# Kernel optimization log

Measured on AMD Instinct MI355X. Metric: run time of the kernel, lower is better.

The kernel has to match this reference:

```python
import jax, jax.numpy as jnp
import numpy as np

# ---- static config (mirrors init_kwargs) ----
B, N, C_IN, C_OUT = 4, 8192, 128, 256
RATIO = 0.25
M = int(N * RATIO)          # sampled centers per cloud (fps ratio)
RADIUS = 0.1
MAX_NN = 64                 # max_num_neighbors
K = 16                      # num kernel points
D_MID = C_IN // 2           # pre_mlp: in_features -> in_features // 2
KP_EXTENT = RADIUS          # kernel-point influence extent (linear influence)


def setup_inputs() -> dict:
    key = jax.random.key(0)
    ks = jax.random.split(key, 10)
    x = jax.random.normal(ks[0], (B, N, C_IN), jnp.float32)
    pos = jax.random.uniform(ks[1], (B, N, 3), jnp.float32)  # unit cube
    W_pre = jax.random.normal(ks[2], (C_IN, D_MID), jnp.float32) / np.sqrt(C_IN).astype(np.float32)
    b_pre = jnp.zeros((D_MID,), jnp.float32)
    kp_pos = jax.random.normal(ks[3], (K, 3), jnp.float32) * (0.3 * RADIUS)
    kp_W = jax.random.normal(ks[4], (K, D_MID, D_MID), jnp.float32) / np.sqrt(D_MID * K).astype(np.float32)
    W_post = jax.random.normal(ks[5], (D_MID, C_OUT), jnp.float32) / np.sqrt(D_MID).astype(np.float32)
    b_post = jnp.zeros((C_OUT,), jnp.float32)
    W_sc = jax.random.normal(ks[6], (C_IN, C_OUT), jnp.float32) / np.sqrt(C_IN).astype(np.float32)
    b_sc = jnp.zeros((C_OUT,), jnp.float32)
    return dict(x=x, pos=pos, W_pre=W_pre, b_pre=b_pre, kp_pos=kp_pos, kp_W=kp_W,
                W_post=W_post, b_post=b_post, W_sc=W_sc, b_sc=b_sc)


def _fps(p):
    """Farthest point sampling on one cloud p:[N,3] -> idx:[M] (start at point 0)."""
    mind = jnp.sum((p - p[0]) ** 2, axis=-1)  # [N]
    def step(mind, _):
        i = jnp.argmax(mind).astype(jnp.int32)
        mind = jnp.minimum(mind, jnp.sum((p - p[i]) ** 2, axis=-1))
        return mind, i
    _, rest = jax.lax.scan(step, mind, None, length=M - 1)
    return jnp.concatenate([jnp.zeros((1,), jnp.int32), rest])


def reference(x, pos, W_pre, b_pre, kp_pos, kp_W, W_post, b_post, W_sc, b_sc):
    def _cloud(xb, pb):
        # xb:[N,C_IN], pb:[N,3]
        idx = _fps(pb)                                   # [M]
        centers = pb[idx]                                # [M,3]
        # radius neighbor search: nearest MAX_NN, mask to ball of RADIUS
        d2 = jnp.sum((centers[:, None, :] - pb[None, :, :]) ** 2, axis=-1)   # [M,N]
        neg_d2, nn_idx = jax.lax.top_k(-d2, MAX_NN)      # [M,MAX_NN]
        valid = (-neg_d2) <= RADIUS ** 2                 # [M,MAX_NN]
        # pre mlp then gather neighbor features (x_j)
        x_pre = xb @ W_pre + b_pre                       # [N,D_MID]
        x_j = x_pre[nn_idx]                              # [M,MAX_NN,D_MID]
        # kernel-point conv: linear influence of each kernel point
        rel = pb[nn_idx] - centers[:, None, :]           # [M,MAX_NN,3]
        dist = jnp.sqrt(jnp.sum((rel[:, :, None, :] - kp_pos[None, None, :, :]) ** 2, axis=-1) + 1e-12)  # [M,MAX_NN,K]
        infl = jnp.maximum(1.0 - dist / KP_EXTENT, 0.0) * valid[:, :, None]
        # aggregate (sum over neighbors) per kernel point, then contract with kernel weights
        s = jnp.einsum('mek,med->mkd', infl, x_j)        # [M,K,D_MID]
        feat = jnp.einsum('mkd,kdo->mo', s, kp_W)        # [M,D_MID]
        feat = feat @ W_post + b_post                    # [M,C_OUT]
        short = xb[idx] @ W_sc + b_sc                    # residual shortcut on sampled points
        return feat + short, centers

    out_feat, out_pos = jax.vmap(_cloud)(x, pos)         # [B,M,C_OUT], [B,M,3]
    return out_feat, out_pos
```

## Files before the change

kernel.cpp:

```cpp
#include <hip/hip_runtime.h>

#define B_    4
#define N_    8192
#define CIN   128
#define COUT  256
#define M_    2048
#define K_    16
#define DM    64
#define MAXNN 64
#define CAP   128
#define R2    0.01f
#define EXT   0.1f

__device__ __forceinline__ float d2_exact(float ax, float ay, float az,
                                          float bx, float by, float bz) {
    float dx = ax - bx, dy = ay - by, dz = az - bz;
    return __fadd_rn(__fadd_rn(__fmul_rn(dx, dx), __fmul_rn(dy, dy)), __fmul_rn(dz, dz));
}

#define DPP_STEP2(CTRL)                                                                   \
    {                                                                                     \
        unsigned tlo = (unsigned)__builtin_amdgcn_update_dpp(0, (int)klo, CTRL, 0xF, 0xF, true); \
        unsigned thi = (unsigned)__builtin_amdgcn_update_dpp(0, (int)khi, CTRL, 0xF, 0xF, true); \
        unsigned long long tk = ((unsigned long long)thi << 32) | tlo;                    \
        unsigned long long ck = ((unsigned long long)khi << 32) | klo;                    \
        if (tk > ck) { klo = tlo; khi = thi; }                                            \
    }

__global__ __launch_bounds__(512) void fps_kernel(const float* __restrict__ pos,
                                                  int* __restrict__ idx_out,
                                                  float* __restrict__ out_pos) {
    const int b = blockIdx.x;
    const int t = threadIdx.x;
    const float* pb = pos + (size_t)b * N_ * 3;

    __shared__ unsigned long long keyS[2][8];

    float px[16], py[16], pz[16], mind[16];
#pragma unroll
    for (int j = 0; j < 16; j++) {
        int n = t + j * 512;
        px[j] = pb[n * 3 + 0];
        py[j] = pb[n * 3 + 1];
        pz[j] = pb[n * 3 + 2];
        mind[j] = 1e30f;
    }
    float cx = pb[0], cy = pb[1], cz = pb[2];
    if (t == 0) {
        idx_out[b * M_ + 0] = 0;
        float* op = out_pos + ((size_t)(b * M_ + 0)) * 3;
        op[0] = cx; op[1] = cy; op[2] = cz;
    }

    for (int m = 1; m < M_; m++) {
        float bv = -1.0f; int bn = 0;
#pragma unroll
        for (int j = 0; j < 16; j++) {
#pragma clang fp contract(off)
            float dx = px[j] - cx, dy = py[j] - cy, dz = pz[j] - cz;
            float d = (dx * dx + dy * dy) + dz * dz;
            d = fminf(mind[j], d);
            mind[j] = d;
            if (d > bv) { bv = d; bn = t + j * 512; }
        }
        unsigned klo = 0xFFFFFFFFu - (unsigned)bn;
        unsigned khi = __float_as_uint(bv);

        DPP_STEP2(0x111)
        DPP_STEP2(0x112)
        DPP_STEP2(0x114)
        DPP_STEP2(0x118)
        DPP_STEP2(0x142)
        DPP_STEP2(0x143)

        const int buf = m & 1;
        if ((t & 63) == 63) {
            keyS[buf][t >> 6] = ((unsigned long long)khi << 32) | klo;
        }
        __syncthreads();
        unsigned long long k0 = keyS[buf][0];
#pragma unroll
        for (int w = 1; w < 8; w++) {
            unsigned long long kw = keyS[buf][w];
            if (kw > k0) k0 = kw;
        }
        const unsigned widx = 0xFFFFFFFFu - (unsigned)(k0 & 0xFFFFFFFFull);
        const float* cp = pb + (size_t)widx * 3;
        cx = cp[0]; cy = cp[1]; cz = cp[2];
        if (t == 0) {
            idx_out[b * M_ + m] = (int)widx;
            float* op = out_pos + ((size_t)(b * M_ + m)) * 3;
            op[0] = cx; op[1] = cy; op[2] = cz;
        }
    }
}

__global__ __launch_bounds__(256) void pre_kernel(const float* __restrict__ x,
                                                  const float* __restrict__ W,
                                                  const float* __restrict__ bvec,
                                                  float* __restrict__ xpre) {
    __shared__ float Ws[CIN * DM];
    __shared__ float xs[16][CIN];
    const int t = threadIdx.x;
    for (int i = t; i < CIN * DM; i += 256) Ws[i] = W[i];
    const size_t rowBase = (size_t)blockIdx.x * 16;
    for (int i = t; i < 16 * CIN; i += 256) {
        int r = i >> 7, c = i & 127;
        xs[r][c] = x[(rowBase + r) * CIN + c];
    }
    __syncthreads();
    const int col = t & 63, r0 = t >> 6;
    float acc[4];
    float bias = bvec[col];
#pragma unroll
    for (int rr = 0; rr < 4; rr++) acc[rr] = bias;
    for (int c = 0; c < CIN; c++) {
        float w = Ws[c * DM + col];
#pragma unroll
        for (int rr = 0; rr < 4; rr++) acc[rr] = fmaf(xs[r0 + 4 * rr][c], w, acc[rr]);
    }
#pragma unroll
    for (int rr = 0; rr < 4; rr++) xpre[(rowBase + r0 + 4 * rr) * DM + col] = acc[rr];
}

__global__ __launch_bounds__(256) void conv_kernel(const float* __restrict__ pos,
                                                   const float* __restrict__ x,
                                                   const float* __restrict__ xpre,
                                                   const int* __restrict__ idxs,
                                                   const float* __restrict__ kp_pos,
                                                   const float* __restrict__ kp_W,
                                                   const float* __restrict__ W_post,
                                                   const float* __restrict__ b_post,
                                                   const float* __restrict__ W_sc,
                                                   const float* __restrict__ b_sc,
                                                   float* __restrict__ out_feat) {
    const int blk = blockIdx.x;
    const int b = blk / M_;
    const int m = blk % M_;
    const int t = threadIdx.x;

    __shared__ int   nIdx[CAP];
    __shared__ float nD2[CAP];
    __shared__ int   cntS;
    __shared__ float infl[MAXNN][K_];
    __shared__ float xj[MAXNN][DM];
    __shared__ float sS[K_ * DM];
    __shared__ float featP[4][DM];
    __shared__ float xg[CIN];

    const float* pb = pos + (size_t)b * N_ * 3;
    const int ctr = idxs[b * M_ + m];
    const float cx = pb[ctr * 3 + 0], cy = pb[ctr * 3 + 1], cz = pb[ctr * 3 + 2];

    if (t == 0) cntS = 0;
    __syncthreads();

    for (int j = 0; j < N_ / 256; j++) {
        int n = j * 256 + t;
        float x0 = pb[n * 3 + 0], y0 = pb[n * 3 + 1], z0 = pb[n * 3 + 2];
        float d = d2_exact(x0, y0, z0, cx, cy, cz);
        if (d <= R2) {
            int p = atomicAdd(&cntS, 1);
            if (p < CAP) { nIdx[p] = n; nD2[p] = d; }
        }
    }
    __syncthreads();
    int cnt = cntS; if (cnt > CAP) cnt = CAP;
    if (cnt > MAXNN) {
        if (t == 0) {
            for (int s = 0; s < MAXNN; s++) {
                int best = s;
                for (int q = s + 1; q < cnt; q++) {
                    if (nD2[q] < nD2[best] || (nD2[q] == nD2[best] && nIdx[q] < nIdx[best])) best = q;
                }
                float td = nD2[best]; nD2[best] = nD2[s]; nD2[s] = td;
                int ti = nIdx[best]; nIdx[best] = nIdx[s]; nIdx[s] = ti;
            }
        }
        __syncthreads();
        cnt = MAXNN;
    }

    if (t < cnt) {
        int n = nIdx[t];
        float rx = pb[n * 3 + 0] - cx, ry = pb[n * 3 + 1] - cy, rz = pb[n * 3 + 2] - cz;
#pragma unroll
        for (int k = 0; k < K_; k++) {
            float dx = rx - kp_pos[k * 3 + 0];
            float dy = ry - kp_pos[k * 3 + 1];
            float dz = rz - kp_pos[k * 3 + 2];
            float dist = sqrtf(dx * dx + dy * dy + dz * dz + 1e-12f);
            infl[t][k] = fmaxf(1.0f - dist / EXT, 0.0f);
        }
    }
    for (int i = t; i < cnt * DM; i += 256) {
        int e = i >> 6, d = i & 63;
        xj[e][d] = xpre[((size_t)b * N_ + nIdx[e]) * DM + d];
    }
    __syncthreads();

#pragma unroll
    for (int p = 0; p < 4; p++) {
        int pair = t + p * 256;
        int k = pair >> 6, d = pair & 63;
        float acc = 0.f;
        for (int e = 0; e < cnt; e++) acc = fmaf(infl[e][k], xj[e][d], acc);
        sS[pair] = acc;
    }
    __syncthreads();

    {
        int dprime = t & 63, ks = t >> 6;
        float acc = 0.f;
        for (int k = ks * 4; k < ks * 4 + 4; k++) {
            const float* kw = kp_W + ((size_t)k * DM) * DM + dprime;
#pragma unroll
            for (int d = 0; d < DM; d++) acc = fmaf(sS[k * DM + d], kw[d * DM], acc);
        }
        featP[ks][dprime] = acc;
    }
    __syncthreads();
    if (t < DM) featP[0][t] = featP[0][t] + featP[1][t] + featP[2][t] + featP[3][t];
    if (t < CIN) xg[t] = x[((size_t)b * N_ + ctr) * CIN + t];
    __syncthreads();

    {
        const int o = t;
        float acc = b_post[o] + b_sc[o];
#pragma unroll 8
        for (int d = 0; d < DM; d++) acc = fmaf(featP[0][d], W_post[d * COUT + o], acc);
#pragma unroll 8
        for (int c = 0; c < CIN; c++) acc = fmaf(xg[c], W_sc[c * COUT + o], acc);
        out_feat[((size_t)(b * M_ + m)) * COUT + o] = acc;
    }
}

extern "C" void kernel_launch(void* const* d_in, const int* in_sizes, int n_in,
                              void* d_out, int out_size, void* d_ws, size_t ws_size,
                              hipStream_t stream) {
    const float* x      = (const float*)d_in[0];
    const float* pos    = (const float*)d_in[1];
    const float* W_pre  = (const float*)d_in[2];
    const float* b_pre  = (const float*)d_in[3];
    const float* kp_pos = (const float*)d_in[4];
    const float* kp_W   = (const float*)d_in[5];
    const float* W_post = (const float*)d_in[6];
    const float* b_post = (const float*)d_in[7];
    const float* W_sc   = (const float*)d_in[8];
    const float* b_sc   = (const float*)d_in[9];

    float* out_feat = (float*)d_out;
    float* out_pos  = (float*)d_out + (size_t)B_ * M_ * COUT;

    int*   idxs = (int*)d_ws;
    float* xpre = (float*)((char*)d_ws + 64 * 1024);

    fps_kernel<<<B_, 512, 0, stream>>>(pos, idxs, out_pos);
    pre_kernel<<<(B_ * N_) / 16, 256, 0, stream>>>(x, W_pre, b_pre, xpre);
    conv_kernel<<<B_ * M_, 256, 0, stream>>>(pos, x, xpre, idxs, kp_pos, kp_W,
                                             W_post, b_post, W_sc, b_sc, out_feat);
}
```

Before: 2.389 ms.

## Fuse pre-MLP into FPS launch, packed-float FPS, atomicMax reduction

Folds the pre-MLP GEMM into the FPS kernel launch as extra blocks, so the pre-MLP runs on idle CUs alongside the four serial FPS blocks and one launch is saved. Inside FPS, the distance update uses 2-wide float vectors, which can map to packed FP32 math. The per-iteration cross-wave reduction now uses a shared atomicMax on a rotating 4-slot buffer instead of eight stores followed by a serial max scan. The risks are LDS atomic contention and the need to reset slots correctly across iterations.

```diff
diff --git a/kernel.cpp b/kernel.cpp
--- a/kernel.cpp
+++ b/kernel.cpp
@@ -12,6 +12,8 @@
 #define R2    0.01f
 #define EXT   0.1f
 
+typedef float v2f __attribute__((ext_vector_type(2)));
+
 __device__ __forceinline__ float d2_exact(float ax, float ay, float az,
                                           float bx, float by, float bz) {
     float dx = ax - bx, dy = ay - by, dz = az - bz;
@@ -27,43 +29,83 @@
         if (tk > ck) { klo = tlo; khi = thi; }                                            \
     }
 
-__global__ __launch_bounds__(512) void fps_kernel(const float* __restrict__ pos,
-                                                  int* __restrict__ idx_out,
-                                                  float* __restrict__ out_pos) {
+__global__ __launch_bounds__(512, 2) void fps_pre_kernel(const float* __restrict__ pos,
+                                                         int* __restrict__ idx_out,
+                                                         float* __restrict__ out_pos,
+                                                         const float* __restrict__ x,
+                                                         const float* __restrict__ Wp,
+                                                         const float* __restrict__ bvec,
+                                                         float* __restrict__ xpre) {
+    __shared__ union {
+        unsigned long long keySlot[4];
+        struct { float Ws[CIN * DM]; float xs[32][CIN]; } p;
+    } sh;
+
+    const int t = threadIdx.x;
+
+    if (blockIdx.x >= 4) {
+        const size_t rowBase = (size_t)(blockIdx.x - 4) * 32;
+        for (int i = t; i < CIN * DM; i += 512) sh.p.Ws[i] = Wp[i];
+        for (int i = t; i < 32 * CIN; i += 512) {
+            int r = i >> 7, c = i & 127;
+            sh.p.xs[r][c] = x[(rowBase + r) * CIN + c];
+        }
+        __syncthreads();
+        const int col = t & 63, r0 = t >> 6;
+        float acc[4];
+        float bias = bvec[col];
+#pragma unroll
+        for (int rr = 0; rr < 4; rr++) acc[rr] = bias;
+        for (int c = 0; c < CIN; c++) {
+            float w = sh.p.Ws[c * DM + col];
+#pragma unroll
+            for (int rr = 0; rr < 4; rr++) acc[rr] = fmaf(sh.p.xs[r0 + 8 * rr][c], w, acc[rr]);
+        }
+#pragma unroll
+        for (int rr = 0; rr < 4; rr++) xpre[(rowBase + r0 + 8 * rr) * DM + col] = acc[rr];
+        return;
+    }
+
     const int b = blockIdx.x;
-    const int t = threadIdx.x;
     const float* pb = pos + (size_t)b * N_ * 3;
 
-    __shared__ unsigned long long keyS[2][8];
-
-    float px[16], py[16], pz[16], mind[16];
-#pragma unroll
-    for (int j = 0; j < 16; j++) {
-        int n = t + j * 512;
-        px[j] = pb[n * 3 + 0];
-        py[j] = pb[n * 3 + 1];
-        pz[j] = pb[n * 3 + 2];
-        mind[j] = 1e30f;
+    v2f px[8], py[8], pz[8], mind[8];
+#pragma unroll
+    for (int jj = 0; jj < 8; jj++) {
+        int n0 = t + (2 * jj) * 512, n1 = n0 + 512;
+        px[jj] = (v2f){pb[n0 * 3 + 0], pb[n1 * 3 + 0]};
+        py[jj] = (v2f){pb[n0 * 3 + 1], pb[n1 * 3 + 1]};
+        pz[jj] = (v2f){pb[n0 * 3 + 2], pb[n1 * 3 + 2]};
+        mind[jj] = (v2f){1e30f, 1e30f};
     }
     float cx = pb[0], cy = pb[1], cz = pb[2];
+    if (t < 4) sh.keySlot[t] = 0ull;
     if (t == 0) {
         idx_out[b * M_ + 0] = 0;
         float* op = out_pos + ((size_t)(b * M_ + 0)) * 3;
         op[0] = cx; op[1] = cy; op[2] = cz;
     }
+    __syncthreads();
 
     for (int m = 1; m < M_; m++) {
-        float bv = -1.0f; int bn = 0;
-#pragma unroll
-        for (int j = 0; j < 16; j++) {
+        float bv = -1.0f; int bj = 0;
+        {
 #pragma clang fp contract(off)
-            float dx = px[j] - cx, dy = py[j] - cy, dz = pz[j] - cz;
-            float d = (dx * dx + dy * dy) + dz * dz;
-            d = fminf(mind[j], d);
-            mind[j] = d;
-            if (d > bv) { bv = d; bn = t + j * 512; }
-        }
-        unsigned klo = 0xFFFFFFFFu - (unsigned)bn;
+            v2f cx2 = (v2f){cx, cx}, cy2 = (v2f){cy, cy}, cz2 = (v2f){cz, cz};
+#pragma unroll
+            for (int jj = 0; jj < 8; jj++) {
+                v2f dx = px[jj] - cx2, dy = py[jj] - cy2, dz = pz[jj] - cz2;
+                v2f d = (dx * dx + dy * dy) + dz * dz;
+                v2f mo = mind[jj];
+                float n0 = fminf(mo.x, d.x);
+                float n1 = fminf(mo.y, d.y);
+                mind[jj] = (v2f){n0, n1};
+                if (n0 > bv) { bv = n0; bj = 2 * jj; }
+                if (n1 > bv) { bv = n1; bj = 2 * jj + 1; }
+            }
+        }
+        const int bn = t + (bj << 9);
+        unsigned klo = ~(unsigned)bn;
         unsigned khi = __float_as_uint(bv);
 
         DPP_STEP2(0x111)
@@ -73,18 +115,14 @@
         DPP_STEP2(0x142)
         DPP_STEP2(0x143)
 
-        const int buf = m & 1;
+        const int buf = m & 3;
         if ((t & 63) == 63) {
-            keyS[buf][t >> 6] = ((unsigned long long)khi << 32) | klo;
+            atomicMax(&sh.keySlot[buf], ((unsigned long long)khi << 32) | klo);
         }
         __syncthreads();
-        unsigned long long k0 = keyS[buf][0];
-#pragma unroll
-        for (int w = 1; w < 8; w++) {
-            unsigned long long kw = keyS[buf][w];
-            if (kw > k0) k0 = kw;
-        }
-        const unsigned widx = 0xFFFFFFFFu - (unsigned)(k0 & 0xFFFFFFFFull);
+        const unsigned long long k0 = sh.keySlot[buf];
+        if (t == 0) sh.keySlot[(m + 2) & 3] = 0ull;
+        const unsigned widx = ~(unsigned)(k0 & 0xFFFFFFFFull);
         const float* cp = pb + (size_t)widx * 3;
         cx = cp[0]; cy = cp[1]; cz = cp[2];
         if (t == 0) {
@@ -93,34 +131,6 @@
             op[0] = cx; op[1] = cy; op[2] = cz;
         }
     }
-}
-
-__global__ __launch_bounds__(256) void pre_kernel(const float* __restrict__ x,
-                                                  const float* __restrict__ W,
-                                                  const float* __restrict__ bvec,
-                                                  float* __restrict__ xpre) {
-    __shared__ float Ws[CIN * DM];
-    __shared__ float xs[16][CIN];
-    const int t = threadIdx.x;
-    for (int i = t; i < CIN * DM; i += 256) Ws[i] = W[i];
-    const size_t rowBase = (size_t)blockIdx.x * 16;
-    for (int i = t; i < 16 * CIN; i += 256) {
-        int r = i >> 7, c = i & 127;
-        xs[r][c] = x[(rowBase + r) * CIN + c];
-    }
-    __syncthreads();
-    const int col = t & 63, r0 = t >> 6;
-    float acc[4];
-    float bias = bvec[col];
-#pragma unroll
-    for (int rr = 0; rr < 4; rr++) acc[rr] = bias;
-    for (int c = 0; c < CIN; c++) {
-        float w = Ws[c * DM + col];
-#pragma unroll
-        for (int rr = 0; rr < 4; rr++) acc[rr] = fmaf(xs[r0 + 4 * rr][c], w, acc[rr]);
-    }
-#pragma unroll
-    for (int rr = 0; rr < 4; rr++) xpre[(rowBase + r0 + 4 * rr) * DM + col] = acc[rr];
 }
 
 __global__ __launch_bounds__(256) void conv_kernel(const float* __restrict__ pos,
@@ -255,8 +265,8 @@
     int*   idxs = (int*)d_ws;
     float* xpre = (float*)((char*)d_ws + 64 * 1024);
 
-    fps_kernel<<<B_, 512, 0, stream>>>(pos, idxs, out_pos);
-    pre_kernel<<<(B_ * N_) / 16, 256, 0, stream>>>(x, W_pre, b_pre, xpre);
+    fps_pre_kernel<<<4 + (B_ * N_) / 32, 512, 0, stream>>>(pos, idxs, out_pos,
+                                                           x, W_pre, b_pre, xpre);
     conv_kernel<<<B_ * M_, 256, 0, stream>>>(pos, x, xpre, idxs, kp_pos, kp_W,
                                              W_post, b_post, W_sc, b_sc, out_feat);
 }
```

After: 2.275 ms. 1.05x faster.
